# Performance work log

Measured on AMD Instinct MI355X. Metric: run time of the kernel, lower is better.

## Reference

```python
import jax, jax.numpy as jnp
import numpy as np

NIBBLE_SHIFTS = jnp.arange(8, dtype=jnp.int32) * 4


def _unpack_int4(packed):
    # packed: [..., P] int32 -> [..., P*8] int32 values in [0, 15]
    vals = (packed[..., None] >> NIBBLE_SHIFTS) & 0xF
    return vals.reshape(*packed.shape[:-1], packed.shape[-1] * 8)


def setup_inputs() -> dict:
    key = jax.random.key(0)
    k1, k2, k3, k4, k5, k6 = jax.random.split(key, 6)
    M, K, N, G = 4096, 4096, 11008, 128
    inp = jax.random.normal(k1, (M, K), dtype=jnp.float32)
    qweight = jax.random.randint(k2, (K, N // 8), 0, 2147483647, dtype=jnp.int32)
    woq_scales = jax.random.uniform(k3, (K // G, N), dtype=jnp.float32)
    woq_qzeros = jax.random.randint(k4, (K // G, N // 8), 0, 2147483647, dtype=jnp.int32)
    woq_bias = jax.random.normal(k5, (N,), dtype=jnp.float32)
    mul = jax.random.normal(k6, (M, N), dtype=jnp.float32)
    return {"inp": inp, "qweight": qweight, "woq_scales": woq_scales,
            "woq_qzeros": woq_qzeros, "woq_bias": woq_bias, "mul": mul,
            "group_size": G}


def reference(inp, qweight, woq_scales, woq_qzeros, woq_bias, mul, group_size):
    K = qweight.shape[0]
    # dequantize int4 weights: w = (q - z) * scale, per group of `group_size` K-rows
    w_int = _unpack_int4(qweight).astype(jnp.float32)            # [K, N]
    z_int = _unpack_int4(woq_qzeros).astype(jnp.float32)         # [K/G, N]
    zeros_full = jnp.repeat(z_int, group_size, axis=0)           # [K, N]
    scales_full = jnp.repeat(woq_scales, group_size, axis=0)     # [K, N]
    w = (w_int - zeros_full) * scales_full                       # [K, N]
    woq_out = inp @ w + woq_bias                                 # [M, N]
    return jax.nn.silu(woq_out) * mul
```

## Files before the change

kernel.cpp:

```cpp
#include <hip/hip_runtime.h>
#include <hip/hip_bf16.h>

typedef __attribute__((ext_vector_type(8))) short short8;
typedef __attribute__((ext_vector_type(4))) short short4v;
typedef __attribute__((ext_vector_type(4))) float float4v;

__device__ __forceinline__ short f2bf(float f) {
  union { float f; unsigned u; } v; v.f = f;
  unsigned r = v.u + 0x7fffu + ((v.u >> 16) & 1u);
  return (short)(r >> 16);
}

typedef const __attribute__((address_space(1))) unsigned int* as1_u32p;
typedef __attribute__((address_space(3))) unsigned int* as3_u32p;

__device__ __forceinline__ void gl_lds16(const void* g, void* l) {
  __builtin_amdgcn_global_load_lds((as1_u32p)g, (as3_u32p)l, 16, 0, 0);
}

__global__ __launch_bounds__(256, 2)
void dequant_kernel(const int* __restrict__ qw,
                    const float* __restrict__ scales,
                    const int* __restrict__ qzeros,
                    short* __restrict__ Bt,
                    int K, int N, int G)
{
  __shared__ short Ls[128 * 64];
  const int N8  = N >> 3;
  const int k0  = blockIdx.x * 64;
  const int n80 = blockIdx.y * 16;
  const int g   = k0 / G;
  const int tid  = threadIdx.x;
  const int lane = tid & 63;
  const int w    = tid >> 6;

  const int4 q4 = *(const int4*)(qw + (size_t)(k0 + lane) * N8 + n80 + w * 4);
  const int4 z4 = *(const int4*)(qzeros + (size_t)g * N8 + n80 + w * 4);
  const int qa[4] = {q4.x, q4.y, q4.z, q4.w};
  const int za[4] = {z4.x, z4.y, z4.z, z4.w};

  #pragma unroll
  for (int it = 0; it < 4; ++it) {
    const int n8l = w * 4 + it;
    const float4v s0 = *(const float4v*)(scales + (size_t)g * N + (n80 + n8l) * 8);
    const float4v s1 = *(const float4v*)(scales + (size_t)g * N + (n80 + n8l) * 8 + 4);
    const float sc[8] = {s0[0], s0[1], s0[2], s0[3], s1[0], s1[1], s1[2], s1[3]};
    const int wq = qa[it], wz = za[it];
    #pragma unroll
    for (int j = 0; j < 8; ++j) {
      const float z = (float)((wz >> (4 * j)) & 0xF);
      const float q = (float)((wq >> (4 * j)) & 0xF);
      Ls[(n8l * 8 + j) * 64 + lane] = f2bf((q - z) * sc[j]);
    }
  }
  __syncthreads();

  #pragma unroll
  for (int it = 0; it < 4; ++it) {
    const int c   = tid + it * 256;
    const int row = c >> 3;
    const int off = (c & 7) * 8;
    const short8 v = *(const short8*)(&Ls[row * 64 + off]);
    *(short8*)(Bt + (size_t)(n80 * 8 + row) * K + k0 + off) = v;
  }
}

__global__ __launch_bounds__(256, 4)
void aconv_kernel(const float* __restrict__ in, short* __restrict__ out, long long n)
{
  const long long i = ((long long)blockIdx.x * blockDim.x + threadIdx.x) * 8;
  if (i >= n) return;
  const float4v a = *(const float4v*)(in + i);
  const float4v b = *(const float4v*)(in + i + 4);
  short8 h;
  h[0] = f2bf(a[0]); h[1] = f2bf(a[1]); h[2] = f2bf(a[2]); h[3] = f2bf(a[3]);
  h[4] = f2bf(b[0]); h[5] = f2bf(b[1]); h[6] = f2bf(b[2]); h[7] = f2bf(b[3]);
  *(short8*)(out + i) = h;
}

__global__ __launch_bounds__(256, 2)
void gemm_silu_mul_kernel(const short* __restrict__ A,
                          const short* __restrict__ Bt,
                          const float* __restrict__ bias,
                          const float* __restrict__ mulp,
                          float*       __restrict__ out,
                          int M, int N, int K)
{
  __shared__ short As[128 * 64];
  __shared__ short Bs[128 * 64];

  const int tid  = threadIdx.x;
  const int lane = tid & 63;
  const int wave = tid >> 6;
  const int wr = (wave >> 1) * 64;
  const int wc = (wave & 1) * 64;
  const int m0 = blockIdx.y * 128;
  const int n0 = blockIdx.x * 128;

  float4v acc[4][4];
  #pragma unroll
  for (int i = 0; i < 4; ++i)
    #pragma unroll
    for (int j = 0; j < 4; ++j)
      acc[i][j] = (float4v){0.f, 0.f, 0.f, 0.f};

  const int fm = lane & 15;
  const int fk = (lane >> 4) * 8;
  const int srow = lane >> 3;
  const int scol = (lane & 7) * 8;

  for (int k0 = 0; k0 < K; k0 += 64) {
    #pragma unroll
    for (int c = 0; c < 4; ++c) {
      const int chunk = wave * 4 + c;
      const int row   = chunk * 8 + srow;
      gl_lds16(A  + (size_t)(m0 + row) * K + k0 + scol, &As[chunk * 512]);
      gl_lds16(Bt + (size_t)(n0 + row) * K + k0 + scol, &Bs[chunk * 512]);
    }
    __syncthreads();

    #pragma unroll
    for (int ks = 0; ks < 64; ks += 32) {
      short8 a[4], b[4];
      #pragma unroll
      for (int mt = 0; mt < 4; ++mt)
        a[mt] = *(const short8*)(&As[(wr + mt * 16 + fm) * 64 + ks + fk]);
      #pragma unroll
      for (int nt = 0; nt < 4; ++nt)
        b[nt] = *(const short8*)(&Bs[(wc + nt * 16 + fm) * 64 + ks + fk]);
      #pragma unroll
      for (int mt = 0; mt < 4; ++mt)
        #pragma unroll
        for (int nt = 0; nt < 4; ++nt)
          acc[mt][nt] = __builtin_amdgcn_mfma_f32_16x16x32_bf16(a[mt], b[nt], acc[mt][nt], 0, 0, 0);
    }
    __syncthreads();
  }

  const int cn = lane & 15;
  const int cr = (lane >> 4) * 4;
  #pragma unroll
  for (int mt = 0; mt < 4; ++mt) {
    #pragma unroll
    for (int nt = 0; nt < 4; ++nt) {
      const int n  = n0 + wc + nt * 16 + cn;
      const float bn = bias[n];
      #pragma unroll
      for (int i = 0; i < 4; ++i) {
        const int m = m0 + wr + mt * 16 + cr + i;
        float x = acc[mt][nt][i] + bn;
        float s = x / (1.0f + __expf(-x));
        out[(size_t)m * N + n] = s * mulp[(size_t)m * N + n];
      }
    }
  }
}

#define BM 128
#define BN 128
#define BK 64
#define LDA 72
#define LDB 72

__global__ __launch_bounds__(256, 2)
void woq_silu_mul_kernel(const float* __restrict__ inp, const int* __restrict__ qw,
                         const float* __restrict__ scales, const int* __restrict__ qzeros,
                         const float* __restrict__ bias, const float* __restrict__ mulp,
                         float* __restrict__ out, int M, int N, int K, int G)
{
  __shared__ short As[BM * LDA];
  __shared__ short Bs[BN * LDB];
  const int tid  = threadIdx.x;
  const int lane = tid & 63;
  const int wave = tid >> 6;
  const int wr = (wave >> 1) * 64;
  const int wc = (wave & 1) * 64;
  const int m0 = blockIdx.y * BM;
  const int n0 = blockIdx.x * BN;
  const int N8 = N >> 3;
  float4v acc[4][4];
  #pragma unroll
  for (int i = 0; i < 4; ++i)
    #pragma unroll
    for (int j = 0; j < 4; ++j)
      acc[i][j] = (float4v){0.f, 0.f, 0.f, 0.f};
  const int n8l  = tid >> 4;
  const int kloc = (tid & 15) * 4;
  const int fm = lane & 15;
  const int fk = (lane >> 4) * 8;
  for (int k0 = 0; k0 < K; k0 += BK) {
    #pragma unroll
    for (int i = 0; i < 8; ++i) {
      int f = tid + i * 256;
      int row = f >> 4;
      int col = (f & 15) * 4;
      float4v a4 = *(const float4v*)(inp + (size_t)(m0 + row) * K + k0 + col);
      short4v h;
      h[0] = f2bf(a4[0]); h[1] = f2bf(a4[1]); h[2] = f2bf(a4[2]); h[3] = f2bf(a4[3]);
      *(short4v*)(&As[row * LDA + col]) = h;
    }
    {
      const int g = k0 / G;
      const int n8g = (n0 >> 3) + n8l;
      const int zw = qzeros[(size_t)g * N8 + n8g];
      const float4v s0 = *(const float4v*)(scales + (size_t)g * N + n0 + n8l * 8);
      const float4v s1 = *(const float4v*)(scales + (size_t)g * N + n0 + n8l * 8 + 4);
      float sc[8] = {s0[0], s0[1], s0[2], s0[3], s1[0], s1[1], s1[2], s1[3]};
      int w[4];
      #pragma unroll
      for (int kk = 0; kk < 4; ++kk)
        w[kk] = qw[(size_t)(k0 + kloc + kk) * N8 + n8g];
      #pragma unroll
      for (int j = 0; j < 8; ++j) {
        const float zj = (float)((w[0], (zw >> (4 * j)) & 0xF));
        const float sj = sc[j];
        short4v h;
        #pragma unroll
        for (int kk = 0; kk < 4; ++kk) {
          int q = (w[kk] >> (4 * j)) & 0xF;
          h[kk] = f2bf(((float)q - zj) * sj);
        }
        *(short4v*)(&Bs[(n8l * 8 + j) * LDB + kloc]) = h;
      }
    }
    __syncthreads();
    #pragma unroll
    for (int ks = 0; ks < BK; ks += 32) {
      short8 a[4], b[4];
      #pragma unroll
      for (int mt = 0; mt < 4; ++mt)
        a[mt] = *(const short8*)(&As[(wr + mt * 16 + fm) * LDA + ks + fk]);
      #pragma unroll
      for (int nt = 0; nt < 4; ++nt)
        b[nt] = *(const short8*)(&Bs[(wc + nt * 16 + fm) * LDB + ks + fk]);
      #pragma unroll
      for (int mt = 0; mt < 4; ++mt)
        #pragma unroll
        for (int nt = 0; nt < 4; ++nt)
          acc[mt][nt] = __builtin_amdgcn_mfma_f32_16x16x32_bf16(a[mt], b[nt], acc[mt][nt], 0, 0, 0);
    }
    __syncthreads();
  }
  const int cn = lane & 15;
  const int cr = (lane >> 4) * 4;
  #pragma unroll
  for (int mt = 0; mt < 4; ++mt) {
    #pragma unroll
    for (int nt = 0; nt < 4; ++nt) {
      const int n = n0 + wc + nt * 16 + cn;
      const float bn = bias[n];
      #pragma unroll
      for (int i = 0; i < 4; ++i) {
        const int m = m0 + wr + mt * 16 + cr + i;
        float x = acc[mt][nt][i] + bn;
        float s = x / (1.0f + __expf(-x));
        out[(size_t)m * N + n] = s * mulp[(size_t)m * N + n];
      }
    }
  }
}

extern "C" void kernel_launch(void* const* d_in, const int* in_sizes, int n_in,
                              void* d_out, int out_size, void* d_ws, size_t ws_size,
                              hipStream_t stream) {
  const float* inp    = (const float*)d_in[0];
  const int*   qw     = (const int*)d_in[1];
  const float* scales = (const float*)d_in[2];
  const int*   qzeros = (const int*)d_in[3];
  const float* bias   = (const float*)d_in[4];
  const float* mulp   = (const float*)d_in[5];
  float*       out    = (float*)d_out;

  const int N = in_sizes[4];
  const int K = (int)(((long long)in_sizes[1] * 8) / N);
  const int M = (int)((long long)in_sizes[0] / K);
  const int G = K / (in_sizes[2] / N);

  const size_t btBytes = (size_t)N * K * sizeof(short);
  const size_t aBytes  = (size_t)M * K * sizeof(short);

  if (ws_size >= btBytes + aBytes) {
    short* Bt  = (short*)d_ws;
    short* Abf = (short*)((char*)d_ws + btBytes);

    dim3 dq_grid(K / 64, (N / 8) / 16);
    dequant_kernel<<<dq_grid, dim3(256), 0, stream>>>(qw, scales, qzeros, Bt, K, N, G);

    const long long nA = (long long)M * K;
    aconv_kernel<<<dim3((unsigned)((nA / 8 + 255) / 256)), dim3(256), 0, stream>>>(inp, Abf, nA);

    dim3 grid(N / 128, M / 128);
    gemm_silu_mul_kernel<<<grid, dim3(256), 0, stream>>>(Abf, Bt, bias, mulp, out, M, N, K);
  } else {
    dim3 grid(N / BN, M / BM);
    woq_silu_mul_kernel<<<grid, dim3(256), 0, stream>>>(inp, qw, scales, qzeros,
                                                        bias, mulp, out, M, N, K, G);
  }
}
```

Measured before the change: 813.6 us.

## Add 256x256-tile GEMM with LDS double buffering and XCD-aware block swizzle

Adds a new 512-thread GEMM kernel that computes 256x256 output tiles. It double-buffers A and B tiles in LDS using direct global-to-LDS loads, prefetching the next K-step while the current one runs MFMA. The kernel remaps block IDs so neighbouring tiles land on the same XCD, uses swizzled LDS offsets, and raises wave priority around the MFMA bursts. Larger tiles cut global and LDS traffic per FLOP and mean fewer blocks, but each block needs about 128KB of LDS, which limits occupancy. A redundant comma expression in the fallback kernel is also cleaned up.

After: 728.0 us. 1.12x faster.

```diff
diff --git a/kernel.cpp b/kernel.cpp
--- a/kernel.cpp
+++ b/kernel.cpp
@@ -76,6 +76,131 @@
   h[0] = f2bf(a[0]); h[1] = f2bf(a[1]); h[2] = f2bf(a[2]); h[3] = f2bf(a[3]);
   h[4] = f2bf(b[0]); h[5] = f2bf(b[1]); h[6] = f2bf(b[2]); h[7] = f2bf(b[3]);
   *(short8*)(out + i) = h;
+}
+
+__global__ __launch_bounds__(512, 2)
+void gemm256_silu_mul_kernel(const short* __restrict__ A,
+                             const short* __restrict__ Bt,
+                             const float* __restrict__ bias,
+                             const float* __restrict__ mulp,
+                             float*       __restrict__ out,
+                             int M, int N, int K)
+{
+  __shared__ short L[2][2][16384];
+
+  const int tid  = threadIdx.x;
+  const int lane = tid & 63;
+  const int wave = tid >> 6;
+  const int wm   = wave >> 2;
+  const int wn   = wave & 3;
+
+  const int nwg = gridDim.x;
+  const int q8 = nwg >> 3, r8 = nwg & 7;
+  const int xcd = blockIdx.x & 7, sub = blockIdx.x >> 3;
+  const int swz = (xcd < r8 ? xcd * (q8 + 1) : r8 * (q8 + 1) + (xcd - r8) * q8) + sub;
+  const int nbx = N >> 8;
+  const int bx = swz % nbx, by = swz / nbx;
+  const int m0 = by << 8, n0 = bx << 8;
+
+  const short* Ab = A  + (size_t)m0 * K;
+  const short* Bb = Bt + (size_t)n0 * K;
+
+  const int srow = lane >> 2;
+  const int scol = (((lane & 3) ^ ((lane & 32) >> 4))) * 8;
+  const int fm = lane & 15;
+  const int ko = ((lane >> 4) * 8) ^ ((fm & 8) ? 16 : 0);
+
+  float4v acc[8][4];
+  #pragma unroll
+  for (int i = 0; i < 8; ++i)
+    #pragma unroll
+    for (int j = 0; j < 4; ++j)
+      acc[i][j] = (float4v){0.f, 0.f, 0.f, 0.f};
+
+  const int NT = K >> 6;
+
+  auto stage = [&](int buf, int ab, const short* __restrict__ base, int kk) {
+    #pragma unroll
+    for (int i = 0; i < 4; ++i) {
+      const int ms = wave * 2 + (i >> 1);
+      const int ks = i & 1;
+      const int st = ms * 2 + ks;
+      gl_lds16(base + (size_t)(ms * 16 + srow) * K + kk + ks * 32 + scol,
+               &L[buf][ab][st * 512]);
+    }
+  };
+
+  stage(0, 0, Ab, 0);
+  stage(0, 1, Bb, 0);
+
+  for (int t = 0; t < NT; ++t) {
+    const int cur = t & 1;
+    const int kk1 = (t + 1) << 6;
+    const bool pf = (t + 1) < NT;
+
+    asm volatile("s_waitcnt vmcnt(0)" ::: "memory");
+    __builtin_amdgcn_s_barrier();
+
+    #pragma unroll
+    for (int qm = 0; qm < 2; ++qm) {
+      short8 af[4][2];
+      #pragma unroll
+      for (int i = 0; i < 4; ++i)
+        #pragma unroll
+        for (int ks = 0; ks < 2; ++ks)
+          af[i][ks] = *(const short8*)(
+              &L[cur][0][((wm * 8 + qm * 4 + i) * 2 + ks) * 512 + fm * 32 + ko]);
+
+      #pragma unroll
+      for (int qn = 0; qn < 2; ++qn) {
+        short8 bf[2][2];
+        #pragma unroll
+        for (int j = 0; j < 2; ++j)
+          #pragma unroll
+          for (int ks = 0; ks < 2; ++ks)
+            bf[j][ks] = *(const short8*)(
+                &L[cur][1][((wn * 4 + qn * 2 + j) * 2 + ks) * 512 + fm * 32 + ko]);
+
+        if (qm == 0 && pf) {
+          if (qn == 0) stage(cur ^ 1, 0, Ab, kk1);
+          else         stage(cur ^ 1, 1, Bb, kk1);
+        }
+
+        __builtin_amdgcn_s_barrier();
+        asm volatile("s_waitcnt lgkmcnt(0)" ::: "memory");
+        __builtin_amdgcn_sched_barrier(0);
+        __builtin_amdgcn_s_setprio(1);
+        #pragma unroll
+        for (int i = 0; i < 4; ++i)
+          #pragma unroll
+          for (int j = 0; j < 2; ++j)
+            #pragma unroll
+            for (int ks = 0; ks < 2; ++ks)
+              acc[qm * 4 + i][qn * 2 + j] = __builtin_amdgcn_mfma_f32_16x16x32_bf16(
+                  af[i][ks], bf[j][ks], acc[qm * 4 + i][qn * 2 + j], 0, 0, 0);
+        __builtin_amdgcn_s_setprio(0);
+        __builtin_amdgcn_s_barrier();
+      }
+    }
+  }
+
+  const int cn  = lane & 15;
+  const int cr4 = (lane >> 4) * 4;
+  #pragma unroll
+  for (int mt = 0; mt < 8; ++mt) {
+    #pragma unroll
+    for (int nt = 0; nt < 4; ++nt) {
+      const int n  = n0 + wn * 64 + nt * 16 + cn;
+      const float bn = bias[n];
+      #pragma unroll
+      for (int i = 0; i < 4; ++i) {
+        const int m = m0 + wm * 128 + mt * 16 + cr4 + i;
+        float x = acc[mt][nt][i] + bn;
+        float s = x / (1.0f + __expf(-x));
+        out[(size_t)m * N + n] = s * mulp[(size_t)m * N + n];
+      }
+    }
+  }
 }
 
 __global__ __launch_bounds__(256, 2)
@@ -212,7 +337,7 @@
         w[kk] = qw[(size_t)(k0 + kloc + kk) * N8 + n8g];
       #pragma unroll
       for (int j = 0; j < 8; ++j) {
-        const float zj = (float)((w[0], (zw >> (4 * j)) & 0xF));
+        const float zj = (float)((zw >> (4 * j)) & 0xF);
         const float sj = sc[j];
         short4v h;
         #pragma unroll
@@ -289,8 +414,13 @@
     const long long nA = (long long)M * K;
     aconv_kernel<<<dim3((unsigned)((nA / 8 + 255) / 256)), dim3(256), 0, stream>>>(inp, Abf, nA);
 
-    dim3 grid(N / 128, M / 128);
-    gemm_silu_mul_kernel<<<grid, dim3(256), 0, stream>>>(Abf, Bt, bias, mulp, out, M, N, K);
+    if ((M & 255) == 0 && (N & 255) == 0 && (K & 63) == 0) {
+      dim3 grid((unsigned)((N >> 8) * (M >> 8)));
+      gemm256_silu_mul_kernel<<<grid, dim3(512), 0, stream>>>(Abf, Bt, bias, mulp, out, M, N, K);
+    } else {
+      dim3 grid(N / 128, M / 128);
+      gemm_silu_mul_kernel<<<grid, dim3(256), 0, stream>>>(Abf, Bt, bias, mulp, out, M, N, K);
+    }
   } else {
     dim3 grid(N / BN, M / BM);
     woq_silu_mul_kernel<<<grid, dim3(256), 0, stream>>>(inp, qw, scales, qzeros,
```
